# Kernel optimization log

Hardware: AMD Instinct MI355X
Metric: run time of the kernel (lower is better)

The kernel has to match this reference:

```python
import jax, jax.numpy as jnp
import numpy as np

DIM = 1024
HEADS = 16
DHEAD = 64
MAXLEN = 512
B = 8
N = 256   # sequence (x) length
M = 256   # memory (h) length; M + N <= MAXLEN
INNER = HEADS * DHEAD


def setup_inputs() -> dict:
    key = jax.random.key(0)
    ks = jax.random.split(key, 8)
    w = lambda k, shape: jax.random.normal(k, shape, jnp.float32) * 0.02
    return {
        "x": jax.random.normal(ks[0], (B, N, DIM), jnp.float32),
        "h": jax.random.normal(ks[1], (B, M, DIM), jnp.float32),
        "Wqkv": w(ks[2], (DIM, 3 * INNER)),
        "Wkr": w(ks[3], (DIM, INNER)),
        "R": jax.random.normal(ks[4], (2 * MAXLEN, DIM), jnp.float32),
        "u": jax.random.normal(ks[5], (DHEAD,), jnp.float32),
        "v": jax.random.normal(ks[6], (DHEAD,), jnp.float32),
        "Wout": w(ks[7], (INNER, DIM)),
        "max_len": MAXLEN,
    }


def reference(x, h, Wqkv, Wkr, R, u, v, Wout, max_len):
    b, n, dim = x.shape
    m = h.shape[1]
    t = m + n
    scale = DHEAD ** -0.5

    cat = jnp.concatenate([h, x], axis=1)                     # [b, t, dim]
    qkv = cat @ Wqkv                                          # [b, t, 3*inner]
    q, k, val = [s.reshape(b, t, HEADS, DHEAD).transpose(0, 2, 1, 3)
                 for s in jnp.split(qkv, 3, axis=-1)]          # [b, h, t, d]

    # shifts[i, j] = (j - i) mod 2L, sliced as in the torch buffer
    ar = jnp.arange(2 * max_len)
    shifts_full = (ar[None, :] - ar[:, None]) % (2 * max_len)
    shifts = shifts_full[:max_len, :max_len][m:m + n, :t]      # [n, t]

    kr = (R @ Wkr)[shifts]                                    # gather: [n, t, inner]
    kr = kr.reshape(n, t, HEADS, DHEAD).transpose(2, 0, 1, 3)  # [h, n, t, d]

    q = q[:, :, m:]                                           # [b, h, n, d]

    term_a = jnp.einsum('bhnd,bhmd->bhnm', q, k)
    term_b = jnp.einsum('bhnd,hnmd->bhnm', q, kr)
    term_c = jnp.einsum('d,bhmd->bhm', u, k)[:, :, None, :]    # broadcast over n
    term_d = jnp.einsum('d,hnmd->hnm', v, kr)[None]            # broadcast over b
    dots = (term_a + term_b + term_c + term_d) * scale         # [b, h, n, t]

    qi = jnp.arange(n)[:, None]
    jm = jnp.arange(m)[None, :]
    js = jnp.arange(n)[None, :]
    mem_mask = jnp.where(qi > jm, -jnp.inf, 0.0)               # [n, m]
    ar_mask = jnp.where(js > qi, -jnp.inf, 0.0)                # [n, n]
    bias = jnp.concatenate([mem_mask, ar_mask], axis=1)[None, None]  # [1,1,n,t]

    attn = jax.nn.softmax(dots + bias, axis=-1)
    out = jnp.einsum('bhnm,bhmd->bhnd', attn, val)             # [b, h, n, d]
    out = out.transpose(0, 2, 1, 3).reshape(b, n, INNER)
    return out @ Wout
```

## Files before the change

kernel.cpp:

```cpp
#include <hip/hip_runtime.h>
#include <hip/hip_bf16.h>
#include <math.h>

typedef unsigned short u16;
typedef short bf16x8 __attribute__((ext_vector_type(8)));
typedef float f32x4 __attribute__((ext_vector_type(4)));

__device__ __forceinline__ u16 f2b(float f) {
    __hip_bfloat16 h = __float2bfloat16(f);
    return *reinterpret_cast<u16*>(&h);
}
__device__ __forceinline__ float b2f(u16 v) {
    __hip_bfloat16 h;
    *reinterpret_cast<u16*>(&h) = v;
    return __bfloat162float(h);
}

__device__ __forceinline__ void gload_lds16(const void* g, void* l) {
    __builtin_amdgcn_global_load_lds(
        (const __attribute__((address_space(1))) void*)g,
        (__attribute__((address_space(3))) void*)l, 16, 0, 0);
}


struct EpiQKV4 {
    u16 *Q, *Kt, *Vt;
    __device__ void operator()(int rowp, int colp, f32x4 vals) const {
        int b = colp >> 9, pos = colp & 511;
        int sec = rowp >> 10, cc = rowp & 1023;
        int head = cc >> 6, d0 = cc & 63;
        ushort4 o;
        if (sec == 0) {
            if (pos < 256) return;
            o.x = f2b(vals[0] * 0.125f); o.y = f2b(vals[1] * 0.125f);
            o.z = f2b(vals[2] * 0.125f); o.w = f2b(vals[3] * 0.125f);
            *(ushort4*)(Q + (long)((head * 8 + b) * 256 + (pos - 256)) * 64 + d0) = o;
        } else {
            u16* dst = (sec == 1) ? Kt : Vt;
            o.x = f2b(vals[0]); o.y = f2b(vals[1]);
            o.z = f2b(vals[2]); o.w = f2b(vals[3]);
            *(ushort4*)(dst + (long)((b * 16 + head) * 512 + pos) * 64 + d0) = o;
        }
    }
};

struct EpiStoreBf {
    u16* C; long ldc; long strideZ;
    __device__ void operator()(int z, int row, int col, float val) const {
        C[(long)z * strideZ + (long)row * ldc + col] = f2b(val);
    }
};

struct EpiStoreF32 {
    float* C; long ldc;
    __device__ void operator()(int z, int row, int col, float val) const {
        C[(long)row * ldc + col] = val;
    }
};


template <typename Epi, bool AF32, bool ADDA, bool ROWMAP>
__device__ __forceinline__ void gemm_bt_body(char* smem, int bx, int by, int bz,
                                             const void* __restrict__ Av, int lda, long strideAz,
                                             const u16* __restrict__ B, int ldb, long strideBz,
                                             int K, Epi epi, const float* __restrict__ av) {
    constexpr int LDT = 56;
    u16* As = (u16*)smem;
    u16* Bs = As + 64 * LDT;
    int n0 = bx * 64, m0 = by * 64, z = bz;
    const u16* Bb = B + (long)z * strideBz + (long)n0 * ldb;
    int tid = threadIdx.x;
    int wave = tid >> 6, lane = tid & 63;
    int wm = wave >> 1, wn = wave & 1;
    int lrow = lane & 15, lquad = lane >> 4;
    int srow = tid >> 2, scol = (tid & 3) * 8;
    f32x4 acc[2][2] = {};
    for (int k0 = 0; k0 < K; k0 += 32) {
        if constexpr (AF32) {
            long arow = m0 + srow;
            if constexpr (ROWMAP) arow = (arow < 256) ? 768 + arow : 0;
            const float* src = (const float*)Av + (long)z * strideAz + arow * lda + k0 + scol;
            float4 f0 = *(const float4*)src;
            float4 f1 = *(const float4*)(src + 4);
            bf16x8 vv;
            vv[0] = (short)f2b(f0.x); vv[1] = (short)f2b(f0.y);
            vv[2] = (short)f2b(f0.z); vv[3] = (short)f2b(f0.w);
            vv[4] = (short)f2b(f1.x); vv[5] = (short)f2b(f1.y);
            vv[6] = (short)f2b(f1.z); vv[7] = (short)f2b(f1.w);
            *(bf16x8*)(As + srow * LDT + scol) = vv;
        } else {
            const u16* Ab = (const u16*)Av + (long)z * strideAz + (long)m0 * lda;
            *(bf16x8*)(As + srow * LDT + scol) = *(const bf16x8*)(Ab + (long)srow * lda + k0 + scol);
        }
        *(bf16x8*)(Bs + srow * LDT + scol) = *(const bf16x8*)(Bb + (long)srow * ldb + k0 + scol);
        __syncthreads();
        bf16x8 af[2], bfr[2];
        #pragma unroll
        for (int mt = 0; mt < 2; ++mt) {
            af[mt] = *(const bf16x8*)(As + (wm * 32 + mt * 16 + lrow) * LDT + lquad * 8);
            if constexpr (ADDA) {
                #pragma unroll
                for (int j = 0; j < 8; ++j)
                    af[mt][j] = (short)f2b(b2f((u16)af[mt][j]) + 0.125f * av[k0 + lquad * 8 + j]);
            }
        }
        #pragma unroll
        for (int nt = 0; nt < 2; ++nt)
            bfr[nt] = *(const bf16x8*)(Bs + (wn * 32 + nt * 16 + lrow) * LDT + lquad * 8);
        #pragma unroll
        for (int mt = 0; mt < 2; ++mt)
            #pragma unroll
            for (int nt = 0; nt < 2; ++nt)
                acc[mt][nt] = __builtin_amdgcn_mfma_f32_16x16x32_bf16(af[mt], bfr[nt], acc[mt][nt], 0, 0, 0);
        __syncthreads();
    }
    #pragma unroll
    for (int mt = 0; mt < 2; ++mt)
        #pragma unroll
        for (int nt = 0; nt < 2; ++nt)
            #pragma unroll
            for (int r = 0; r < 4; ++r) {
                int row = m0 + wm * 32 + mt * 16 + lquad * 4 + r;
                int col = n0 + wn * 32 + nt * 16 + lrow;
                epi(z, row, col, acc[mt][nt][r]);
            }
}

__global__ __launch_bounds__(256) void prep_kernel(const float* __restrict__ x,
                                                   const float* __restrict__ h,
                                                   u16* __restrict__ catBF,
                                                   const float* __restrict__ Wqkv, u16* __restrict__ WqkvT,
                                                   const float* __restrict__ Wkr,  u16* __restrict__ WkrT,
                                                   const float* __restrict__ Wout, u16* __restrict__ WoutT) {
    __shared__ float tile[32][33];
    int bid = blockIdx.x, tid = threadIdx.x;
    if (bid < 2048) {
        int idx = (bid * 256 + tid) * 8;
        int c = idx & 1023, r = idx >> 10;
        int b = r >> 9, pos = r & 511;
        const float* src = (pos < 256) ? h + ((long)(b * 256 + pos) * 1024 + c)
                                       : x + ((long)(b * 256 + pos - 256) * 1024 + c);
        float4 f0 = *(const float4*)src;
        float4 f1 = *(const float4*)(src + 4);
        bf16x8 vv;
        vv[0] = (short)f2b(f0.x); vv[1] = (short)f2b(f0.y);
        vv[2] = (short)f2b(f0.z); vv[3] = (short)f2b(f0.w);
        vv[4] = (short)f2b(f1.x); vv[5] = (short)f2b(f1.y);
        vv[6] = (short)f2b(f1.z); vv[7] = (short)f2b(f1.w);
        *(bf16x8*)(catBF + idx) = vv;
        return;
    }
    const float* W; u16* WT; int nb, kb;
    if (bid < 5120) {
        int w = bid - 2048;
        W = Wqkv; WT = WqkvT;
        nb = (w % 96) * 32; kb = (w / 96) * 32;
        int tx = tid & 31, ty = tid >> 5;
        #pragma unroll
        for (int i = 0; i < 32; i += 8)
            tile[ty + i][tx] = W[(long)(kb + ty + i) * 3072 + nb + tx];
    } else {
        int w = bid - 5120;
        if (w < 1024) { W = Wkr; WT = WkrT; }
        else          { W = Wout; WT = WoutT; w -= 1024; }
        nb = (w & 31) * 32; kb = (w >> 5) * 32;
        int tx = tid & 31, ty = tid >> 5;
        #pragma unroll
        for (int i = 0; i < 32; i += 8)
            tile[ty + i][tx] = W[(long)(kb + ty + i) * 1024 + nb + tx];
    }
    __syncthreads();
    int row = tid >> 3;
    int c4 = (tid & 7) * 4;
    ushort4 o;
    o.x = f2b(tile[c4 + 0][row]);
    o.y = f2b(tile[c4 + 1][row]);
    o.z = f2b(tile[c4 + 2][row]);
    o.w = f2b(tile[c4 + 3][row]);
    *(ushort4*)(WT + (long)(nb + row) * 1024 + kb + c4) = o;
}

__global__ __launch_bounds__(256) void qkv_rwg_kernel(const u16* __restrict__ A, const u16* __restrict__ B,
                                                      EpiQKV4 eq,
                                                      const float* __restrict__ R, const u16* __restrict__ WkrT,
                                                      u16* __restrict__ RWg) {
    __shared__ alignas(16) char smem[65536];
    int bid0 = blockIdx.x;
    if (bid0 >= 640) {
        int bid2 = bid0 - 640;
        gemm_bt_body<EpiStoreBf, true, false, true>(smem, bid2 & 15, bid2 >> 4, 0,
            (const void*)R, 1024, 0L, WkrT, 1024, 0L, 1024, EpiStoreBf{RWg, 1024, 0}, nullptr);
        return;
    }
    int bid = (bid0 & 7) * 80 + (bid0 >> 3);
    int m0, n0;
    if (bid < 512) {
        m0 = 1024 + (bid >> 5) * 128;
        n0 = (bid & 31) * 128;
    } else {
        int q = bid - 512;
        m0 = (q >> 4) * 128;
        int c = q & 15;
        n0 = (c >> 1) * 512 + 256 + (c & 1) * 128;
    }
    int tid = threadIdx.x, wave = tid >> 6, lane = tid & 63;
    int wm = wave >> 1, wn = wave & 1;
    int lrow = lane & 15, lquad = lane >> 4;
    const u16* Ab = A + (long)m0 * 1024;
    const u16* Bb = B + (long)n0 * 1024;
    f32x4 acc[4][4] = {};

    auto stage = [&](int buf, int k0) {
        u16* Asb = (u16*)smem + buf * 16384;
        u16* Bsb = Asb + 8192;
        #pragma unroll
        for (int i = 0; i < 4; ++i) {
            int rowb = (i & 1) * 64 + (tid >> 2);
            int col = k0 + (i >> 1) * 32 + (tid & 3) * 8;
            gload_lds16(Ab + (long)rowb * 1024 + col, Asb + i * 2048 + tid * 8);
            gload_lds16(Bb + (long)rowb * 1024 + col, Bsb + i * 2048 + tid * 8);
        }
    };
    auto compute = [&](int buf) {
        u16* Asb = (u16*)smem + buf * 16384;
        u16* Bsb = Asb + 8192;
        #pragma unroll
        for (int ks = 0; ks < 2; ++ks) {
            bf16x8 af[4], bfr[4];
            #pragma unroll
            for (int mt = 0; mt < 4; ++mt)
                af[mt] = *(const bf16x8*)(Asb + ks * 4096 + (wm * 64 + mt * 16 + lrow) * 32 + lquad * 8);
            #pragma unroll
            for (int nt = 0; nt < 4; ++nt)
                bfr[nt] = *(const bf16x8*)(Bsb + ks * 4096 + (wn * 64 + nt * 16 + lrow) * 32 + lquad * 8);
            #pragma unroll
            for (int mt = 0; mt < 4; ++mt)
                #pragma unroll
                for (int nt = 0; nt < 4; ++nt)
                    acc[mt][nt] = __builtin_amdgcn_mfma_f32_16x16x32_bf16(af[mt], bfr[nt], acc[mt][nt], 0, 0, 0);
        }
    };

    stage(0, 0);
    stage(1, 64);
    for (int t = 0; t < 15; ++t) {
        asm volatile("s_waitcnt vmcnt(8)" ::: "memory");
        __builtin_amdgcn_sched_barrier(0);
        __builtin_amdgcn_s_barrier();
        __builtin_amdgcn_sched_barrier(0);
        compute(t & 1);
        __builtin_amdgcn_sched_barrier(0);
        __builtin_amdgcn_s_barrier();
        __builtin_amdgcn_sched_barrier(0);
        if (t < 14) stage(t & 1, (t + 2) * 64);
    }
    asm volatile("s_waitcnt vmcnt(0)" ::: "memory");
    __builtin_amdgcn_sched_barrier(0);
    __builtin_amdgcn_s_barrier();
    __builtin_amdgcn_sched_barrier(0);
    compute(1);

    #pragma unroll
    for (int mt = 0; mt < 4; ++mt)
        #pragma unroll
        for (int nt = 0; nt < 4; ++nt) {
            int rowp = m0 + wm * 64 + mt * 16 + lquad * 4;
            int colp = n0 + wn * 64 + nt * 16 + lrow;
            eq(rowp, colp, acc[mt][nt]);
        }
}

__global__ __launch_bounds__(256) void vtrans_qr_kernel(const u16* __restrict__ Vtmp, u16* __restrict__ VT,
                                                        const u16* __restrict__ Q, const u16* __restrict__ RWg,
                                                        u16* __restrict__ QR, const float* __restrict__ v) {
    __shared__ alignas(16) char smem[14336];
    int bid = blockIdx.x, tid = threadIdx.x;
    if (bid < 4096) {
        u16 (*tile)[34] = (u16(*)[34])smem;
        int t0 = (bid & 15) * 32, d0 = ((bid >> 4) & 1) * 32, bh = bid >> 5;
        int tx = tid & 31, ty = tid >> 5;
        const u16* src = Vtmp + (long)bh * 512 * 64;
        #pragma unroll
        for (int i = 0; i < 32; i += 8)
            tile[ty + i][tx] = src[(long)(t0 + ty + i) * 64 + d0 + tx];
        __syncthreads();
        u16* dst = VT + (long)bh * 64 * 512;
        #pragma unroll
        for (int i = 0; i < 32; i += 8)
            dst[(long)(d0 + ty + i) * 512 + t0 + tx] = tile[tx][ty + i];
        return;
    }
    int bid2 = bid - 4096;
    int bx = bid2 % 5;
    int rest = bid2 / 5;
    int by = rest & 31, bz = rest >> 5;
    gemm_bt_body<EpiStoreBf, false, true, false>(smem, bx, by, bz,
        (const void*)Q, 64, 2048L * 64, RWg, 1024, 64L, 64,
        EpiStoreBf{QR, 320, 2048L * 320}, v);
}

__global__ __launch_bounds__(256) void outproj_kernel(const u16* __restrict__ A,
                                                      const u16* __restrict__ B,
                                                      float* __restrict__ out) {
    __shared__ alignas(16) char smem[14336];
    gemm_bt_body<EpiStoreF32, false, false, false>(smem, blockIdx.x, blockIdx.y, 0,
        (const void*)A, 1024, 0L, B, 1024, 0L, 1024, EpiStoreF32{out, 1024}, nullptr);
}

__global__ __launch_bounds__(256, 4) void attn_kernel(const u16* __restrict__ Qs,
                                                      const u16* __restrict__ Kt,
                                                      const u16* __restrict__ VT,
                                                      const u16* __restrict__ QR,
                                                      const float* __restrict__ uvec,
                                                      u16* __restrict__ attnOut) {
    constexpr int LDSW = 328;
    __shared__ alignas(16) u16 SQ[32 * LDSW];
    __shared__ float red[2][4][32];
    int id = blockIdx.x;
    int bh = id & 127, it = id >> 7;
    int b = bh >> 4, h = bh & 15;
    int i0 = it * 32;
    int w0 = i0;
    int tid = threadIdx.x, wave = tid >> 6, lane = tid & 63;
    int lrow = lane & 15, lquad = lane >> 4;

    const u16* qrg = QR + ((long)h * 2048 + b * 256 + i0) * 320;
    #pragma unroll
    for (int kk = 0; kk < 5; ++kk) {
        int idx = tid + kk * 256;
        int row = idx / 40, c = idx - row * 40;
        *(bf16x8*)(SQ + row * LDSW + c * 8) = *(const bf16x8*)(qrg + row * 320 + c * 8);
    }

    bf16x8 aq[2][2];
    #pragma unroll
    for (int iu = 0; iu < 2; ++iu) {
        const u16* qbase = Qs + (long)((h * 8 + b) * 256 + i0 + iu * 16 + lrow) * 64;
        aq[iu][0] = *(const bf16x8*)(qbase + lquad * 8);
        aq[iu][1] = *(const bf16x8*)(qbase + 32 + lquad * 8);
        #pragma unroll
        for (int j = 0; j < 8; ++j) {
            aq[iu][0][j] = (short)f2b(b2f((u16)aq[iu][0][j]) + 0.125f * uvec[lquad * 8 + j]);
            aq[iu][1][j] = (short)f2b(b2f((u16)aq[iu][1][j]) + 0.125f * uvec[32 + lquad * 8 + j]);
        }
    }

    const u16* kbase = Kt + ((long)bh * 512 + w0 + wave * 80) * 64;
    bf16x8 bk0[5], bk1[5];
    #pragma unroll
    for (int t = 0; t < 5; ++t) {
        const u16* kp = kbase + (long)(t * 16 + lrow) * 64;
        bk0[t] = *(const bf16x8*)(kp + lquad * 8);
        bk1[t] = *(const bf16x8*)(kp + 32 + lquad * 8);
    }
    f32x4 acc[2][5];
    #pragma unroll
    for (int t = 0; t < 5; ++t)
        #pragma unroll
        for (int iu = 0; iu < 2; ++iu) {
            f32x4 a = {0.f, 0.f, 0.f, 0.f};
            a = __builtin_amdgcn_mfma_f32_16x16x32_bf16(aq[iu][0], bk0[t], a, 0, 0, 0);
            a = __builtin_amdgcn_mfma_f32_16x16x32_bf16(aq[iu][1], bk1[t], a, 0, 0, 0);
            acc[iu][t] = a;
        }
    __syncthreads();

    float m4[2][4];
    #pragma unroll
    for (int iu = 0; iu < 2; ++iu)
        #pragma unroll
        for (int r = 0; r < 4; ++r) m4[iu][r] = -1e30f;
    #pragma unroll
    for (int t = 0; t < 5; ++t) {
        int lj = wave * 80 + t * 16 + lrow;
        #pragma unroll
        for (int iu = 0; iu < 2; ++iu)
            #pragma unroll
            for (int r = 0; r < 4; ++r) {
                int rloc = iu * 16 + lquad * 4 + r;
                int d = lj - rloc;
                int dc = d < 0 ? 0 : (d > 256 ? 256 : d);
                bool ok = (unsigned)d <= 256u;
                float val = ok ? acc[iu][t][r] + b2f(SQ[rloc * LDSW + dc]) : -1e30f;
                acc[iu][t][r] = val;
                m4[iu][r] = fmaxf(m4[iu][r], val);
            }
    }
    #pragma unroll
    for (int iu = 0; iu < 2; ++iu)
        #pragma unroll
        for (int r = 0; r < 4; ++r) {
            #pragma unroll
            for (int off = 1; off < 16; off <<= 1)
                m4[iu][r] = fmaxf(m4[iu][r], __shfl_xor(m4[iu][r], off));
            if (lrow == 0) red[0][wave][iu * 16 + lquad * 4 + r] = m4[iu][r];
        }
    __syncthreads();

    float gmax[2][4];
    #pragma unroll
    for (int iu = 0; iu < 2; ++iu)
        #pragma unroll
        for (int r = 0; r < 4; ++r) {
            int row = iu * 16 + lquad * 4 + r;
            gmax[iu][r] = fmaxf(fmaxf(red[0][0][row], red[0][1][row]),
                                fmaxf(red[0][2][row], red[0][3][row]));
        }

    float s4[2][4] = {};
    #pragma unroll
    for (int t = 0; t < 5; ++t) {
        int lj = wave * 80 + t * 16 + lrow;
        #pragma unroll
        for (int iu = 0; iu < 2; ++iu)
            #pragma unroll
            for (int r = 0; r < 4; ++r) {
                float p = __expf(acc[iu][t][r] - gmax[iu][r]);
                s4[iu][r] += p;
                SQ[(iu * 16 + lquad * 4 + r) * LDSW + lj] = f2b(p);
            }
    }
    #pragma unroll
    for (int iu = 0; iu < 2; ++iu)
        #pragma unroll
        for (int r = 0; r < 4; ++r) {
            #pragma unroll
            for (int off = 1; off < 16; off <<= 1)
                s4[iu][r] += __shfl_xor(s4[iu][r], off);
            if (lrow == 0) red[1][wave][iu * 16 + lquad * 4 + r] = s4[iu][r];
        }
    __syncthreads();

    const u16* vbase = VT + ((long)bh * 64 + wave * 16 + lrow) * 512 + w0;
    f32x4 oacc[2] = {};
    bf16x8 vp[10];
    #pragma unroll
    for (int t = 0; t < 10; ++t)
        vp[t] = *(const bf16x8*)(vbase + t * 32 + lquad * 8);
    #pragma unroll
    for (int t = 0; t < 10; ++t)
        #pragma unroll
        for (int iu = 0; iu < 2; ++iu) {
            bf16x8 ap = *(const bf16x8*)(SQ + (iu * 16 + lrow) * LDSW + t * 32 + lquad * 8);
            oacc[iu] = __builtin_amdgcn_mfma_f32_16x16x32_bf16(ap, vp[t], oacc[iu], 0, 0, 0);
        }
    #pragma unroll
    for (int iu = 0; iu < 2; ++iu)
        #pragma unroll
        for (int r = 0; r < 4; ++r) {
            int row = iu * 16 + lquad * 4 + r;
            float inv = 1.0f / (red[1][0][row] + red[1][1][row] + red[1][2][row] + red[1][3][row]);
            attnOut[(long)(b * 256 + i0 + row) * 1024 + h * 64 + wave * 16 + lrow] = f2b(oacc[iu][r] * inv);
        }
}


extern "C" void kernel_launch(void* const* d_in, const int* in_sizes, int n_in,
                              void* d_out, int out_size, void* d_ws, size_t ws_size,
                              hipStream_t stream) {
    (void)in_sizes; (void)n_in; (void)out_size; (void)ws_size;
    const float* x    = (const float*)d_in[0];
    const float* h    = (const float*)d_in[1];
    const float* Wqkv = (const float*)d_in[2];
    const float* Wkr  = (const float*)d_in[3];
    const float* R    = (const float*)d_in[4];
    const float* u    = (const float*)d_in[5];
    const float* v    = (const float*)d_in[6];
    const float* Wout = (const float*)d_in[7];
    float* out = (float*)d_out;

    char* ws = (char*)d_ws;
    size_t off = 0;
    auto alloc = [&](size_t bytes) -> void* {
        void* p = ws + off;
        off = (off + bytes + 255) & ~(size_t)255;
        return p;
    };
    u16* catBF  = (u16*)alloc(4096L * 1024 * 2);
    u16* WqkvT  = (u16*)alloc(3072L * 1024 * 2);
    u16* WkrT   = (u16*)alloc(1024L * 1024 * 2);
    u16* WoutT  = (u16*)alloc(1024L * 1024 * 2);
    u16* RWg    = (u16*)alloc(320L * 1024 * 2);
    u16* Q      = (u16*)alloc(16L * 8 * 256 * 64 * 2);
    u16* Kt     = (u16*)alloc(8L * 16 * 512 * 64 * 2);
    u16* Vtmp   = (u16*)alloc(8L * 16 * 512 * 64 * 2);
    u16* VT     = (u16*)alloc(8L * 16 * 64 * 512 * 2);
    u16* QR     = (u16*)alloc(16L * 2048 * 320 * 2);
    u16* attnO  = (u16*)alloc(2048L * 1024 * 2);

    prep_kernel<<<7168, 256, 0, stream>>>(x, h, catBF, Wqkv, WqkvT, Wkr, WkrT, Wout, WoutT);
    qkv_rwg_kernel<<<720, 256, 0, stream>>>(WqkvT, catBF, EpiQKV4{Q, Kt, Vtmp}, R, WkrT, RWg);
    vtrans_qr_kernel<<<6656, 256, 0, stream>>>(Vtmp, VT, Q, RWg, QR, v);
    attn_kernel<<<1024, 256, 0, stream>>>(Q, Kt, VT, QR, u, attnO);
    outproj_kernel<<<dim3(16, 32), 256, 0, stream>>>(attnO, WoutT, out);
}
```

Measured before the change: 185.6 us.

## Halve QKV GEMM K-tile for higher occupancy and regroup blocks per XCD

The QKV GEMM's K step drops from 64 to 32, which halves the LDS buffer to 32KB and lets launch bounds request 4 blocks per SIMD group. The main loop now runs 31 iterations with a smaller vmcnt wait. Block indices are also remapped so each XCD handles groups of 8 adjacent N-tiles that share one M-row, to improve L2 reuse of A. The cost is twice as many barriers per K and fewer MFMAs between syncs. There is also a risk that the R@Wkr branch's gemm_bt_body expects more than 32KB of shared memory.

```diff
diff --git a/kernel.cpp b/kernel.cpp
--- a/kernel.cpp
+++ b/kernel.cpp
@@ -180,11 +180,11 @@
     *(ushort4*)(WT + (long)(nb + row) * 1024 + kb + c4) = o;
 }
 
-__global__ __launch_bounds__(256) void qkv_rwg_kernel(const u16* __restrict__ A, const u16* __restrict__ B,
-                                                      EpiQKV4 eq,
-                                                      const float* __restrict__ R, const u16* __restrict__ WkrT,
-                                                      u16* __restrict__ RWg) {
-    __shared__ alignas(16) char smem[65536];
+__global__ __launch_bounds__(256, 4) void qkv_rwg_kernel(const u16* __restrict__ A, const u16* __restrict__ B,
+                                                         EpiQKV4 eq,
+                                                         const float* __restrict__ R, const u16* __restrict__ WkrT,
+                                                         u16* __restrict__ RWg) {
+    __shared__ alignas(16) char smem[32768];
     int bid0 = blockIdx.x;
     if (bid0 >= 640) {
         int bid2 = bid0 - 640;
@@ -192,15 +192,19 @@
             (const void*)R, 1024, 0L, WkrT, 1024, 0L, 1024, EpiStoreBf{RWg, 1024, 0}, nullptr);
         return;
     }
-    int bid = (bid0 & 7) * 80 + (bid0 >> 3);
+    int xcd = bid0 & 7, s = bid0 >> 3;
+    int G = xcd * 10 + (s >> 3);
+    int w = s & 7;
     int m0, n0;
-    if (bid < 512) {
-        m0 = 1024 + (bid >> 5) * 128;
-        n0 = (bid & 31) * 128;
+    if (G < 64) {
+        int nchunk = G >> 4, mrow = G & 15;
+        m0 = 1024 + mrow * 128;
+        n0 = (nchunk * 8 + w) * 128;
     } else {
-        int q = bid - 512;
-        m0 = (q >> 4) * 128;
-        int c = q & 15;
+        int G2 = G - 64;
+        int nchunk = G2 >> 3, mrow = G2 & 7;
+        m0 = mrow * 128;
+        int c = nchunk * 8 + w;
         n0 = (c >> 1) * 512 + 256 + (c & 1) * 128;
     }
     int tid = threadIdx.x, wave = tid >> 6, lane = tid & 63;
@@ -211,40 +215,37 @@
     f32x4 acc[4][4] = {};
 
     auto stage = [&](int buf, int k0) {
-        u16* Asb = (u16*)smem + buf * 16384;
-        u16* Bsb = Asb + 8192;
-        #pragma unroll
-        for (int i = 0; i < 4; ++i) {
-            int rowb = (i & 1) * 64 + (tid >> 2);
-            int col = k0 + (i >> 1) * 32 + (tid & 3) * 8;
+        u16* Asb = (u16*)smem + buf * 8192;
+        u16* Bsb = Asb + 4096;
+        #pragma unroll
+        for (int i = 0; i < 2; ++i) {
+            int rowb = i * 64 + (tid >> 2);
+            int col = k0 + (tid & 3) * 8;
             gload_lds16(Ab + (long)rowb * 1024 + col, Asb + i * 2048 + tid * 8);
             gload_lds16(Bb + (long)rowb * 1024 + col, Bsb + i * 2048 + tid * 8);
         }
     };
     auto compute = [&](int buf) {
-        u16* Asb = (u16*)smem + buf * 16384;
-        u16* Bsb = Asb + 8192;
-        #pragma unroll
-        for (int ks = 0; ks < 2; ++ks) {
-            bf16x8 af[4], bfr[4];
-            #pragma unroll
-            for (int mt = 0; mt < 4; ++mt)
-                af[mt] = *(const bf16x8*)(Asb + ks * 4096 + (wm * 64 + mt * 16 + lrow) * 32 + lquad * 8);
+        u16* Asb = (u16*)smem + buf * 8192;
+        u16* Bsb = Asb + 4096;
+        bf16x8 af[4], bfr[4];
+        #pragma unroll
+        for (int mt = 0; mt < 4; ++mt)
+            af[mt] = *(const bf16x8*)(Asb + (wm * 64 + mt * 16 + lrow) * 32 + lquad * 8);
+        #pragma unroll
+        for (int nt = 0; nt < 4; ++nt)
+            bfr[nt] = *(const bf16x8*)(Bsb + (wn * 64 + nt * 16 + lrow) * 32 + lquad * 8);
+        #pragma unroll
+        for (int mt = 0; mt < 4; ++mt)
             #pragma unroll
             for (int nt = 0; nt < 4; ++nt)
-                bfr[nt] = *(const bf16x8*)(Bsb + ks * 4096 + (wn * 64 + nt * 16 + lrow) * 32 + lquad * 8);
-            #pragma unroll
-            for (int mt = 0; mt < 4; ++mt)
-                #pragma unroll
-                for (int nt = 0; nt < 4; ++nt)
-                    acc[mt][nt] = __builtin_amdgcn_mfma_f32_16x16x32_bf16(af[mt], bfr[nt], acc[mt][nt], 0, 0, 0);
-        }
+                acc[mt][nt] = __builtin_amdgcn_mfma_f32_16x16x32_bf16(af[mt], bfr[nt], acc[mt][nt], 0, 0, 0);
     };
 
     stage(0, 0);
-    stage(1, 64);
-    for (int t = 0; t < 15; ++t) {
-        asm volatile("s_waitcnt vmcnt(8)" ::: "memory");
+    stage(1, 32);
+    for (int t = 0; t < 31; ++t) {
+        asm volatile("s_waitcnt vmcnt(4)" ::: "memory");
         __builtin_amdgcn_sched_barrier(0);
         __builtin_amdgcn_s_barrier();
         __builtin_amdgcn_sched_barrier(0);
@@ -252,7 +253,7 @@
         __builtin_amdgcn_sched_barrier(0);
         __builtin_amdgcn_s_barrier();
         __builtin_amdgcn_sched_barrier(0);
-        if (t < 14) stage(t & 1, (t + 2) * 64);
+        if (t < 30) stage(t & 1, (t + 2) * 32);
     }
     asm volatile("s_waitcnt vmcnt(0)" ::: "memory");
     __builtin_amdgcn_sched_barrier(0);
```

New measurement: 177.5 us. -4.4%, faster.
